# Optimization experiments

Hardware: AMD Instinct MI355X
Metric: run time of the kernel (lower is better)

Reference implementation:

```python
import jax, jax.numpy as jnp
import numpy as np

K = 20  # fixed in __init__
BN_EPS = 1e-5


def knn_idx(x, k):
    # x: [B, C, N] -> idx [B, N, k] of k nearest neighbors (largest negative sq-dist)
    xt = jnp.swapaxes(x, 1, 2)                       # [B, N, C]
    inner = -2.0 * jnp.einsum('bnc,bcm->bnm', xt, x)  # [B, N, N]
    xx = jnp.sum(x * x, axis=1, keepdims=True)        # [B, 1, N]
    pd = -xx - inner - jnp.swapaxes(xx, 1, 2)         # negative squared distance
    return jax.lax.top_k(pd, k)[1]


def graph_feature(x, k):
    # x: [B, C, N] -> edge features [B, 2C, N, k] = cat(nbr - center, center)
    idx = knn_idx(x, k)                               # [B, N, k]
    xt = jnp.swapaxes(x, 1, 2)                        # [B, N, C]
    nbr = jax.vmap(lambda f, i: f[i])(xt, idx)        # [B, N, k, C] irregular gather
    ctr = jnp.broadcast_to(xt[:, :, None, :], nbr.shape)
    feat = jnp.concatenate([nbr - ctr, ctr], axis=-1)  # [B, N, k, 2C]
    return jnp.transpose(feat, (0, 3, 1, 2))


def bn_apply(y, p):
    # p: [4, C] rows = (gamma, beta, running_mean, running_var); eval-mode BN
    g, b, m, v = p[0], p[1], p[2], p[3]
    shp = (1, -1) + (1,) * (y.ndim - 2)
    return (y - m.reshape(shp)) * (g.reshape(shp) * jax.lax.rsqrt(v.reshape(shp) + BN_EPS)) + b.reshape(shp)


def edge_conv(x, W, p, k):
    # get_graph_feature -> Conv2d 1x1 (no bias) -> BN2d -> LeakyReLU(0.2) -> max over k
    f = graph_feature(x, k)                           # [B, 2C, N, k]
    y = jnp.einsum('oc,bcnk->bonk', W, f)             # 1x1 conv
    y = jax.nn.leaky_relu(bn_apply(y, p), 0.2)
    return jnp.max(y, axis=-1)                        # [B, O, N]


def setup_inputs() -> dict:
    key = jax.random.key(0)
    ks = jax.random.split(key, 6)
    B, C, N = 2, 3, 8192

    def kaiming(k_, out_c, in_c):
        # kaiming_normal fan_out, leaky_relu(0.2): gain = sqrt(2/(1+0.2^2))
        std = (2.0 / (1.0 + 0.2 ** 2) / out_c) ** 0.5
        return (jax.random.normal(k_, (out_c, in_c)) * std).astype(jnp.float32)

    def bnp(c):
        # init: gamma=1, beta=0, running_mean=0, running_var=1
        return jnp.stack([jnp.ones(c), jnp.zeros(c), jnp.zeros(c), jnp.ones(c)]).astype(jnp.float32)

    return {
        'x': jax.random.normal(ks[0], (B, C, N), dtype=jnp.float32),
        'W1': kaiming(ks[1], 64, 2 * C),
        'W2': kaiming(ks[2], 64, 128),
        'W3': kaiming(ks[3], 128, 128),
        'W4': kaiming(ks[4], 256, 256),
        'W5': kaiming(ks[5], 512, 512),
        'bn1': bnp(64), 'bn2': bnp(64), 'bn3': bnp(128), 'bn4': bnp(256), 'bn5': bnp(512),
    }


def reference(x, W1, W2, W3, W4, W5, bn1, bn2, bn3, bn4, bn5):
    x1 = edge_conv(x, W1, bn1, K)    # [B, 64, N]
    x2 = edge_conv(x1, W2, bn2, K)   # [B, 64, N]
    x3 = edge_conv(x2, W3, bn3, K)   # [B, 128, N]
    x4 = edge_conv(x3, W4, bn4, K)   # [B, 256, N]
    cat = jnp.concatenate([x1, x2, x3, x4], axis=1)  # [B, 512, N]
    y = jnp.einsum('oc,bcn->bon', W5, cat)           # conv5 1x1 (no bias)
    return jax.nn.leaky_relu(bn_apply(y, bn5), 0.2)  # [B, 512, N]
```

## Files before the change

### kernel.cpp

```cpp
#include <hip/hip_runtime.h>
#include <stdint.h>

#define NPTS 8192
#define BATCH 2
#define KNN 20
#define BN_EPS 1e-5f

__global__ __launch_bounds__(256) void k_xt(const float* __restrict__ x,
                                            float* __restrict__ xt,
                                            float* __restrict__ nrm) {
  int i = blockIdx.x * 256 + threadIdx.x;
  int b = i / NPTS, n = i % NPTS;
  float x0 = x[((size_t)b * 3 + 0) * NPTS + n];
  float x1 = x[((size_t)b * 3 + 1) * NPTS + n];
  float x2 = x[((size_t)b * 3 + 2) * NPTS + n];
  float4 v = make_float4(x0, x1, x2, 0.f);
  reinterpret_cast<float4*>(xt)[i] = v;
  float s0 = x0 * x0, s1 = x1 * x1, s2 = x2 * x2;
  nrm[i] = (s0 + s1) + s2;
}

__global__ __launch_bounds__(256) void k_prep(const float* __restrict__ W,
                                              float* __restrict__ A2,
                                              int O, int Creal, int Cpad) {
  int i = blockIdx.x * 256 + threadIdx.x;
  if (i >= O * Cpad) return;
  int o = i / Cpad, c = i % Cpad;
  float wn = (c < Creal) ? W[(size_t)o * 2 * Creal + c] : 0.f;
  float wc = (c < Creal) ? W[(size_t)o * 2 * Creal + Creal + c] : 0.f;
  A2[(size_t)o * Cpad + c] = wn;
  A2[(size_t)(O + o) * Cpad + c] = wc - wn;
}

template <int C>
__global__ __launch_bounds__(256) void k_tr(const float* __restrict__ X,
                                            int S, int coff,
                                            float4* __restrict__ XT,
                                            float* __restrict__ nrm) {
  constexpr int C4 = C / 4;
  constexpr int CP = C + 1;
  __shared__ float s[64 * CP];
  const int b = blockIdx.y;
  const int n0 = blockIdx.x * 64;
  const int tid = threadIdx.x;

  for (int v = tid; v < 64 * C; v += 256) {
    int r = v / C, c = v % C;
    s[r * CP + c] = X[(size_t)(b * NPTS + n0 + r) * S + coff + c];
  }
  __syncthreads();

  if (tid < 64) {
    float sum = 0.f;
    const float* row = &s[tid * CP];
#pragma unroll
    for (int c4 = 0; c4 < C4; ++c4) {
      float vx = row[4 * c4 + 0], vy = row[4 * c4 + 1];
      float vz = row[4 * c4 + 2], vw = row[4 * c4 + 3];
      sum = fmaf(vx, vx, sum); sum = fmaf(vy, vy, sum);
      sum = fmaf(vz, vz, sum); sum = fmaf(vw, vw, sum);
    }
    nrm[b * NPTS + n0 + tid] = sum;
  }

  for (int v = tid; v < 64 * C4; v += 256) {
    int c4 = v >> 6, jn = v & 63;
    const float* row = &s[jn * CP + 4 * c4];
    XT[((size_t)b * C4 + c4) * NPTS + n0 + jn] =
        make_float4(row[0], row[1], row[2], row[3]);
  }
}

template <int C>
__global__ __launch_bounds__(256) void k_knn(const float* __restrict__ Xrow,
                                             const float4* __restrict__ XT,
                                             const float* __restrict__ nrm,
                                             int S, int coff,
                                             int* __restrict__ idxout) {
  constexpr int C4 = C / 4;
  constexpr int CH = (C4 < 4) ? C4 : 4;
  constexpr int ROWS = 16;
  __shared__ __align__(16) float s_xi[ROWS * C];
  __shared__ float s_ni[ROWS];
  __shared__ unsigned long long s_list[ROWS * KNN];

  const int b = blockIdx.y;
  const int rowbase = blockIdx.x * ROWS;
  const int tid = threadIdx.x, wave = tid >> 6, lane = tid & 63;

  for (int v = tid; v < ROWS * KNN; v += 256) s_list[v] = ~0ull;
  for (int v = tid; v < ROWS * C; v += 256) {
    int r = v / C, c = v % C;
    s_xi[v] = Xrow[(size_t)(b * NPTS + rowbase + r) * S + coff + c];
  }
  if (tid < ROWS) s_ni[tid] = nrm[b * NPTS + rowbase + tid];
  __syncthreads();

  const int r0 = wave * 4;
  const float4* xbase = XT + (size_t)b * C4 * NPTS;

  for (int jt = 0; jt < NPTS; jt += 64) {
    const int j = jt + lane;
    const float nj = nrm[b * NPTS + j];

    float a[4][4];
#pragma unroll
    for (int r = 0; r < 4; ++r)
      a[r][0] = a[r][1] = a[r][2] = a[r][3] = 0.f;

#pragma unroll 1
    for (int cc = 0; cc < C4; cc += CH) {
      float4 xj[CH];
#pragma unroll
      for (int u = 0; u < CH; ++u)
        xj[u] = xbase[(size_t)(cc + u) * NPTS + j];
#pragma unroll
      for (int u = 0; u < CH; ++u) {
#pragma unroll
        for (int r = 0; r < 4; ++r) {
          float4 v = *reinterpret_cast<const float4*>(
              &s_xi[(r0 + r) * C + 4 * (cc + u)]);
          a[r][0] = fmaf(v.x, xj[u].x, a[r][0]);
          a[r][1] = fmaf(v.y, xj[u].y, a[r][1]);
          a[r][2] = fmaf(v.z, xj[u].z, a[r][2]);
          a[r][3] = fmaf(v.w, xj[u].w, a[r][3]);
        }
      }
    }

#pragma unroll
    for (int r = 0; r < 4; ++r) {
      float dot = (a[r][0] + a[r][1]) + (a[r][2] + a[r][3]);
      float t2 = fmaf(2.f, dot, -s_ni[r0 + r]);
      float d = nj - t2;
      unsigned u = __float_as_uint(d);
      u ^= (unsigned)(((int)u) >> 31) | 0x80000000u;
      unsigned long long key = ((unsigned long long)u << 32) | (unsigned)j;

      unsigned long long* lp = &s_list[(r0 + r) * KNN];
      unsigned long long thr = lp[KNN - 1];
      unsigned long long mask = __ballot(key < thr);
      while (mask) {
        int src = __ffsll((long long)mask) - 1;
        unsigned long long ck = __shfl(key, src);
        unsigned long long e = (lane < KNN) ? lp[lane] : ~0ull;
        unsigned long long ep = __shfl_up(e, 1);
        bool cc2 = ck < e;
        bool cp = (lane > 0) && (ck < ep);
        unsigned long long ne = cp ? ep : (cc2 ? ck : e);
        if (lane < KNN) lp[lane] = ne;
        thr = __shfl(ne, KNN - 1);
        if (lane == src) key = ~0ull;
        mask = __ballot(key < thr);
      }
    }
  }

  if (lane < KNN) {
#pragma unroll
    for (int r = 0; r < 4; ++r)
      idxout[(size_t)(b * NPTS + rowbase + r0 + r) * KNN + lane] =
          (int)(s_list[(r0 + r) * KNN + lane] & 0xffffffffull);
  }
}

__global__ __launch_bounds__(256) void k_gemm(const float* __restrict__ A,
                                              const float* __restrict__ X,
                                              float* __restrict__ Y,
                                              int S, int coff, int C, int O2) {
  __shared__ __align__(16) float sX[16 * 68];
  __shared__ __align__(16) float sA[16 * 68];
  const int b = blockIdx.z;
  const int nb = blockIdx.x * 64;
  const int ob = blockIdx.y * 64;
  const int tid = threadIdx.x, ty = tid >> 4, tx = tid & 15;
  float acc[4][4] = {};

  for (int kc = 0; kc < C; kc += 16) {
#pragma unroll
    for (int t = 0; t < 4; ++t) {
      int v = tid + t * 256;
      int p = v >> 4, k = v & 15;
      float xv = 0.f, av = 0.f;
      if (kc + k < C) {
        xv = X[(size_t)(b * NPTS + nb + p) * S + coff + kc + k];
        av = A[(size_t)(ob + p) * C + kc + k];
      }
      sX[k * 68 + p] = xv;
      sA[k * 68 + p] = av;
    }
    __syncthreads();
#pragma unroll
    for (int kk = 0; kk < 16; ++kk) {
      float4 xa = *reinterpret_cast<const float4*>(&sX[kk * 68 + ty * 4]);
      float4 wb = *reinterpret_cast<const float4*>(&sA[kk * 68 + tx * 4]);
      acc[0][0] = fmaf(xa.x, wb.x, acc[0][0]);
      acc[0][1] = fmaf(xa.x, wb.y, acc[0][1]);
      acc[0][2] = fmaf(xa.x, wb.z, acc[0][2]);
      acc[0][3] = fmaf(xa.x, wb.w, acc[0][3]);
      acc[1][0] = fmaf(xa.y, wb.x, acc[1][0]);
      acc[1][1] = fmaf(xa.y, wb.y, acc[1][1]);
      acc[1][2] = fmaf(xa.y, wb.z, acc[1][2]);
      acc[1][3] = fmaf(xa.y, wb.w, acc[1][3]);
      acc[2][0] = fmaf(xa.z, wb.x, acc[2][0]);
      acc[2][1] = fmaf(xa.z, wb.y, acc[2][1]);
      acc[2][2] = fmaf(xa.z, wb.z, acc[2][2]);
      acc[2][3] = fmaf(xa.z, wb.w, acc[2][3]);
      acc[3][0] = fmaf(xa.w, wb.x, acc[3][0]);
      acc[3][1] = fmaf(xa.w, wb.y, acc[3][1]);
      acc[3][2] = fmaf(xa.w, wb.z, acc[3][2]);
      acc[3][3] = fmaf(xa.w, wb.w, acc[3][3]);
    }
    __syncthreads();
  }
#pragma unroll
  for (int i = 0; i < 4; ++i) {
    float4 st = make_float4(acc[i][0], acc[i][1], acc[i][2], acc[i][3]);
    *reinterpret_cast<float4*>(
        &Y[(size_t)(b * NPTS + nb + ty * 4 + i) * O2 + ob + tx * 4]) = st;
  }
}

__global__ __launch_bounds__(256) void k_gather(const float* __restrict__ UV,
                                                const int* __restrict__ idx,
                                                const float* __restrict__ bn,
                                                float* __restrict__ Xcat,
                                                int O2, int O, int coff_out) {
  const int b = blockIdx.z;
  const int og = blockIdx.y * 64;
  const int wave = threadIdx.x >> 6, lane = threadIdx.x & 63;
  const int n = blockIdx.x * 4 + wave;
  const int o = og + lane;
  const int* ip = &idx[(size_t)(b * NPTS + n) * KNN];
  float g = bn[o], be = bn[O + o], mu = bn[2 * O + o], va = bn[3 * O + o];
  float a = g / sqrtf(va + BN_EPS);
  float cb = be - mu * a;
  float vmax = -3.4e38f, vmin = 3.4e38f;
#pragma unroll
  for (int k = 0; k < KNN; ++k) {
    int jn = ip[k];
    float v = UV[(size_t)(b * NPTS + jn) * O2 + o];
    vmax = fmaxf(vmax, v);
    vmin = fminf(vmin, v);
  }
  float Vc = UV[(size_t)(b * NPTS + n) * O2 + O + o];
  float M = ((a >= 0.f) ? vmax : vmin) + Vc;
  float z = fmaf(a, M, cb);
  Xcat[(size_t)(b * NPTS + n) * 512 + coff_out + o] = fmaxf(z, 0.2f * z);
}

__global__ __launch_bounds__(256) void k_out(const float* __restrict__ Y,
                                             const float* __restrict__ bn,
                                             float* __restrict__ out) {
  int n = blockIdx.x * 256 + threadIdx.x;
  int o = blockIdx.y;
  int b = blockIdx.z;
  float g = bn[o], be = bn[512 + o], mu = bn[1024 + o], va = bn[1536 + o];
  float a = g / sqrtf(va + BN_EPS);
  float cb = be - mu * a;
  float y = Y[(size_t)(b * NPTS + n) * 512 + o];
  float z = fmaf(a, y, cb);
  out[(size_t)(b * 512 + o) * NPTS + n] = fmaxf(z, 0.2f * z);
}

extern "C" void kernel_launch(void* const* d_in, const int* in_sizes, int n_in,
                              void* d_out, int out_size, void* d_ws,
                              size_t ws_size, hipStream_t stream) {
  const float* x  = (const float*)d_in[0];
  const float* W1 = (const float*)d_in[1];
  const float* W2 = (const float*)d_in[2];
  const float* W3 = (const float*)d_in[3];
  const float* W4 = (const float*)d_in[4];
  const float* W5 = (const float*)d_in[5];
  const float* bn1 = (const float*)d_in[6];
  const float* bn2 = (const float*)d_in[7];
  const float* bn3 = (const float*)d_in[8];
  const float* bn4 = (const float*)d_in[9];
  const float* bn5 = (const float*)d_in[10];
  float* out = (float*)d_out;

  float* f    = (float*)d_ws;
  float* xt   = f;
  float* nrm  = f + 65536;
  int*   idx  = (int*)(f + 81920);
  float* Xcat = f + 409600;
  float* UV   = f + 8798208;
  float* A2   = f + 17186816;

  float4* XT = (float4*)UV;

  k_xt<<<64, 256, 0, stream>>>(x, xt, nrm);

  k_prep<<<1, 256, 0, stream>>>(W1, A2, 64, 3, 4);
  k_knn<4><<<dim3(512, 2), 256, 0, stream>>>(xt, (const float4*)xt, nrm, 4, 0, idx);
  k_gemm<<<dim3(128, 2, 2), 256, 0, stream>>>(A2, xt, UV, 4, 0, 4, 128);
  k_gather<<<dim3(2048, 1, 2), 256, 0, stream>>>(UV, idx, bn1, Xcat, 128, 64, 0);

  k_tr<64><<<dim3(128, 2), 256, 0, stream>>>(Xcat, 512, 0, XT, nrm);
  k_prep<<<16, 256, 0, stream>>>(W2, A2, 64, 64, 64);
  k_knn<64><<<dim3(512, 2), 256, 0, stream>>>(Xcat, XT, nrm, 512, 0, idx);
  k_gemm<<<dim3(128, 2, 2), 256, 0, stream>>>(A2, Xcat, UV, 512, 0, 64, 128);
  k_gather<<<dim3(2048, 1, 2), 256, 0, stream>>>(UV, idx, bn2, Xcat, 128, 64, 64);

  k_tr<64><<<dim3(128, 2), 256, 0, stream>>>(Xcat, 512, 64, XT, nrm);
  k_prep<<<32, 256, 0, stream>>>(W3, A2, 128, 64, 64);
  k_knn<64><<<dim3(512, 2), 256, 0, stream>>>(Xcat, XT, nrm, 512, 64, idx);
  k_gemm<<<dim3(128, 4, 2), 256, 0, stream>>>(A2, Xcat, UV, 512, 64, 64, 256);
  k_gather<<<dim3(2048, 2, 2), 256, 0, stream>>>(UV, idx, bn3, Xcat, 256, 128, 128);

  k_tr<128><<<dim3(128, 2), 256, 0, stream>>>(Xcat, 512, 128, XT, nrm);
  k_prep<<<128, 256, 0, stream>>>(W4, A2, 256, 128, 128);
  k_knn<128><<<dim3(512, 2), 256, 0, stream>>>(Xcat, XT, nrm, 512, 128, idx);
  k_gemm<<<dim3(128, 8, 2), 256, 0, stream>>>(A2, Xcat, UV, 512, 128, 128, 512);
  k_gather<<<dim3(2048, 4, 2), 256, 0, stream>>>(UV, idx, bn4, Xcat, 512, 256, 256);

  k_gemm<<<dim3(128, 8, 2), 256, 0, stream>>>(W5, Xcat, UV, 512, 0, 512, 512);
  k_out<<<dim3(32, 512, 2), 256, 0, stream>>>(UV, bn5, out);
}
```

Baseline: 2.835 ms.

## Split kNN candidate range across blocks and merge partial top-k lists

The kNN kernel now splits the candidate point range into two halves via a new grid dimension. Each block writes its partial sorted top-20 keys to a workspace buffer, and a new merge kernel combines the two sorted lists into final indices. This doubles block count to improve GPU occupancy (1024 to 2048 blocks) and halves each block's serial scan length. The cost is an extra kernel launch and extra global traffic for the partial lists, and layer 1 still runs unsplit with a trivial merge.

New measurement: 3.154 ms. 1.11x slower.

```diff
diff --git a/kernel.cpp b/kernel.cpp
--- a/kernel.cpp
+++ b/kernel.cpp
@@ -76,7 +76,7 @@
                                              const float4* __restrict__ XT,
                                              const float* __restrict__ nrm,
                                              int S, int coff,
-                                             int* __restrict__ idxout) {
+                                             unsigned long long* __restrict__ kout) {
   constexpr int C4 = C / 4;
   constexpr int CH = (C4 < 4) ? C4 : 4;
   constexpr int ROWS = 16;
@@ -84,9 +84,12 @@
   __shared__ float s_ni[ROWS];
   __shared__ unsigned long long s_list[ROWS * KNN];
 
-  const int b = blockIdx.y;
+  const int b = blockIdx.z;
   const int rowbase = blockIdx.x * ROWS;
   const int tid = threadIdx.x, wave = tid >> 6, lane = tid & 63;
+  const int nsp = gridDim.y;
+  const int jspan = NPTS / nsp;
+  const int jbase = blockIdx.y * jspan;
 
   for (int v = tid; v < ROWS * KNN; v += 256) s_list[v] = ~0ull;
   for (int v = tid; v < ROWS * C; v += 256) {
@@ -99,7 +102,7 @@
   const int r0 = wave * 4;
   const float4* xbase = XT + (size_t)b * C4 * NPTS;
 
-  for (int jt = 0; jt < NPTS; jt += 64) {
+  for (int jt = jbase; jt < jbase + jspan; jt += 64) {
     const int j = jt + lane;
     const float nj = nrm[b * NPTS + j];
 
@@ -159,8 +162,27 @@
   if (lane < KNN) {
 #pragma unroll
     for (int r = 0; r < 4; ++r)
-      idxout[(size_t)(b * NPTS + rowbase + r0 + r) * KNN + lane] =
-          (int)(s_list[(r0 + r) * KNN + lane] & 0xffffffffull);
+      kout[((size_t)(b * NPTS + rowbase + r0 + r) * nsp + blockIdx.y) * KNN +
+           lane] = s_list[(r0 + r) * KNN + lane];
+  }
+}
+
+__global__ __launch_bounds__(256) void k_merge(
+    const unsigned long long* __restrict__ kbuf, int nsplit,
+    int* __restrict__ idxout) {
+  int row = blockIdx.x * 256 + threadIdx.x;
+  const unsigned long long* kp = kbuf + (size_t)row * nsplit * KNN;
+  int* op = idxout + (size_t)row * KNN;
+  int p0 = 0, p1 = 0;
+#pragma unroll
+  for (int k = 0; k < KNN; ++k) {
+    unsigned long long v0 = (p0 < KNN) ? kp[p0] : ~0ull;
+    unsigned long long v1 =
+        (nsplit > 1 && p1 < KNN) ? kp[KNN + p1] : ~0ull;
+    bool t0 = v0 <= v1;
+    op[k] = (int)((t0 ? v0 : v1) & 0xffffffffull);
+    p0 += t0 ? 1 : 0;
+    p1 += t0 ? 0 : 1;
   }
 }
 
@@ -288,29 +310,34 @@
   float* A2   = f + 17186816;
 
   float4* XT = (float4*)UV;
+  unsigned long long* kbuf = (unsigned long long*)(UV + 3145728);
 
   k_xt<<<64, 256, 0, stream>>>(x, xt, nrm);
 
   k_prep<<<1, 256, 0, stream>>>(W1, A2, 64, 3, 4);
-  k_knn<4><<<dim3(512, 2), 256, 0, stream>>>(xt, (const float4*)xt, nrm, 4, 0, idx);
+  k_knn<4><<<dim3(512, 1, 2), 256, 0, stream>>>(xt, (const float4*)xt, nrm, 4, 0, kbuf);
+  k_merge<<<64, 256, 0, stream>>>(kbuf, 1, idx);
   k_gemm<<<dim3(128, 2, 2), 256, 0, stream>>>(A2, xt, UV, 4, 0, 4, 128);
   k_gather<<<dim3(2048, 1, 2), 256, 0, stream>>>(UV, idx, bn1, Xcat, 128, 64, 0);
 
   k_tr<64><<<dim3(128, 2), 256, 0, stream>>>(Xcat, 512, 0, XT, nrm);
   k_prep<<<16, 256, 0, stream>>>(W2, A2, 64, 64, 64);
-  k_knn<64><<<dim3(512, 2), 256, 0, stream>>>(Xcat, XT, nrm, 512, 0, idx);
+  k_knn<64><<<dim3(512, 2, 2), 256, 0, stream>>>(Xcat, XT, nrm, 512, 0, kbuf);
+  k_merge<<<64, 256, 0, stream>>>(kbuf, 2, idx);
   k_gemm<<<dim3(128, 2, 2), 256, 0, stream>>>(A2, Xcat, UV, 512, 0, 64, 128);
   k_gather<<<dim3(2048, 1, 2), 256, 0, stream>>>(UV, idx, bn2, Xcat, 128, 64, 64);
 
   k_tr<64><<<dim3(128, 2), 256, 0, stream>>>(Xcat, 512, 64, XT, nrm);
   k_prep<<<32, 256, 0, stream>>>(W3, A2, 128, 64, 64);
-  k_knn<64><<<dim3(512, 2), 256, 0, stream>>>(Xcat, XT, nrm, 512, 64, idx);
+  k_knn<64><<<dim3(512, 2, 2), 256, 0, stream>>>(Xcat, XT, nrm, 512, 64, kbuf);
+  k_merge<<<64, 256, 0, stream>>>(kbuf, 2, idx);
   k_gemm<<<dim3(128, 4, 2), 256, 0, stream>>>(A2, Xcat, UV, 512, 64, 64, 256);
   k_gather<<<dim3(2048, 2, 2), 256, 0, stream>>>(UV, idx, bn3, Xcat, 256, 128, 128);
 
   k_tr<128><<<dim3(128, 2), 256, 0, stream>>>(Xcat, 512, 128, XT, nrm);
   k_prep<<<128, 256, 0, stream>>>(W4, A2, 256, 128, 128);
-  k_knn<128><<<dim3(512, 2), 256, 0, stream>>>(Xcat, XT, nrm, 512, 128, idx);
+  k_knn<128><<<dim3(512, 2, 2), 256, 0, stream>>>(Xcat, XT, nrm, 512, 128, kbuf);
+  k_merge<<<64, 256, 0, stream>>>(kbuf, 2, idx);
   k_gemm<<<dim3(128, 8, 2), 256, 0, stream>>>(A2, Xcat, UV, 512, 128, 128, 512);
   k_gather<<<dim3(2048, 4, 2), 256, 0, stream>>>(UV, idx, bn4, Xcat, 512, 256, 256);
 
```
